# Kernel tuning notes

Measured on AMD Instinct MI355X. Metric: run time of the kernel, lower is better.

## Reference

```python
import jax, jax.numpy as jnp
import numpy as np

CUTOFF = 5.0
MAX_NBR = 32      # max_num_neighbors
LOOP = True
B, M = 128, 1024  # molecules, atoms per molecule (batch is uniform: batch[i] = i // M)
BOX = 26.0        # box side chosen so ~30 atoms fall within CUTOFF


def setup_inputs() -> dict:
    key = jax.random.key(0)
    pos = jax.random.uniform(key, (B * M, 3), dtype=jnp.float32) * BOX
    batch = jnp.repeat(jnp.arange(B, dtype=jnp.int32), M)
    return {"pos": pos, "batch": batch}


def reference(pos, batch):
    # radius_graph with per-graph (molecule) candidate search. Equal-size
    # molecules (batch = arange // M) let us use a dense [B, M, M] candidate
    # matrix per molecule; truncation keeps the K nearest within cutoff
    # (PyG keeps an arbitrary K within cutoff; nearest-K is the deterministic
    # variant). Output has fixed shape [2, B*M*K] padded with self-loops.
    posb = pos.reshape(B, M, 3)
    sq = jnp.sum(posb * posb, axis=-1)                       # [B, M]
    dot = jnp.einsum('bmd,bnd->bmn', posb, posb)             # [B, M, M]
    d2 = jnp.maximum(sq[:, :, None] + sq[:, None, :] - 2.0 * dot, 0.0)
    within = d2 <= CUTOFF * CUTOFF
    if not LOOP:
        within = within & ~jnp.eye(M, dtype=bool)[None]
    neg = jnp.where(within, -d2, -jnp.inf)
    vals, idx = jax.lax.top_k(neg, MAX_NBR)                  # [B, M, K]
    valid = jnp.isfinite(vals)
    center = jnp.arange(M, dtype=idx.dtype)[None, :, None]   # [1, M, 1]
    idx_eff = jnp.where(valid, idx, center)                  # pad invalid -> self

    b_ix = jnp.arange(B)[:, None, None]
    nbr = posb[b_ix, idx_eff]                                # [B, M, K, 3]
    edge_vec = nbr - posb[:, :, None, :]                     # pos[src] - pos[dst]

    is_self = idx_eff == center
    wmask = valid & ~is_self                                 # self-loops get weight 0
    d2sel = jnp.sum(edge_vec * edge_vec, axis=-1)
    edge_weight = jnp.where(wmask, jnp.sqrt(jnp.where(wmask, d2sel, 1.0)), 0.0)

    offs = (jnp.arange(B, dtype=idx.dtype) * M)[:, None, None]
    src = (offs + idx_eff).reshape(-1)                       # neighbor (edge_index[0])
    dst = jnp.broadcast_to(offs + center, (B, M, MAX_NBR)).reshape(-1)
    edge_index = jnp.stack([src, dst])                       # [2, B*M*K]
    return edge_index, edge_weight.reshape(-1), edge_vec.reshape(-1, 3)
```

## Files before the change

kernel.cpp:

```cpp
#include <hip/hip_runtime.h>

#define NB 128
#define NM 1024
#define NK 32
#define NS 16
#define CUT2 25.0f
#define CUT2_BITS 0x41C80000u
#define KEYMASK   0xFFFFFC00u

typedef unsigned int   u32;
typedef unsigned short u16;
typedef float vf4 __attribute__((ext_vector_type(4)));

__global__ __launch_bounds__(256) void pack_atoms(const float* __restrict__ pos,
                                                  float4* __restrict__ scanb,
                                                  float4* __restrict__ rawb, int dual)
{
  int i = blockIdx.x * 256 + threadIdx.x;
  float x = pos[3*i+0], y = pos[3*i+1], z = pos[3*i+2];
  float sq = x*x + y*y + z*z;
  rawb[i] = make_float4(x, y, z, sq);
  if (dual) scanb[i] = make_float4(-2.f*x, -2.f*y, -2.f*z, sq);
}

__device__ __forceinline__ void ce_asc(u32 &a, u32 &b) {
  u32 mn = a < b ? a : b;
  u32 mx = a < b ? b : a;
  a = mn; b = mx;
}

template <int N, int K, int D>
__device__ __forceinline__ void bitonic_pass(u32* r) {
#pragma unroll
  for (int i = 0; i < N; ++i)
    if ((i & D) == 0) {
      if ((i & K) == 0) ce_asc(r[i], r[i | D]);
      else              ce_asc(r[i | D], r[i]);
    }
}

template <bool NEG2>
__global__ __launch_bounds__(256, 4) void radius_knn(const float4* __restrict__ scanb,
                                                     const float4* __restrict__ rawb,
                                                     float* __restrict__ out)
{
  __shared__ float xs[NM], ys[NM], zs[NM], sqs[NM];
  __shared__ u32 lmem[4096];
  u16* lists = (u16*)lmem;

  const int tid  = threadIdx.x;
  const int lane = tid & 127;
  const int half = tid >> 7;
  const int molb = blockIdx.x & 127;
  const int q8   = blockIdx.x >> 7;
  const int c    = molb * NM + q8 * 128 + lane;
  const int mloc = c & (NM - 1);

  const float4* st = rawb + (size_t)molb * NM;
  for (int t = tid; t < NM; t += 256) {
    float4 a = st[t];
    xs[t] = a.x; ys[t] = a.y; zs[t] = a.z; sqs[t] = a.w;
  }
  __syncthreads();

  const float mex = xs[mloc], mey = ys[mloc], mez = zs[mloc], mew = sqs[mloc];

  const float4* mp = scanb + ((size_t)(c >> 10) << 10);
  const int jbase = half * 512;
  int cnt = 0;
  float4 ta[8], tb[8];
#pragma unroll
  for (int u = 0; u < 8; ++u) ta[u] = mp[jbase + u];

  auto body = [&](const float4* t, int j0) {
#pragma unroll
    for (int u = 0; u < 8; ++u) {
      float d2;
      if (NEG2) {
        d2 = __builtin_fmaf(mex, t[u].x,
             __builtin_fmaf(mey, t[u].y,
             __builtin_fmaf(mez, t[u].z, mew + t[u].w)));
      } else {
        float dot = (mex*t[u].x + mey*t[u].y) + mez*t[u].z;
        d2 = __builtin_fmaf(-2.f, dot, mew + t[u].w);
      }
      int slot = cnt < NS ? cnt : (NS - 1);
      lists[slot * 256 + tid] = (u16)(j0 + u);
      cnt += (d2 <= CUT2) ? 1 : 0;
    }
  };

  for (int g = 0; g < 64; g += 2) {
    const int j1 = jbase + (((g + 1) & 63) << 3);
#pragma unroll
    for (int u = 0; u < 8; ++u) tb[u] = mp[j1 + u];
    body(ta, jbase + (g << 3));
    const int j2 = jbase + (((g + 2) & 63) << 3);
#pragma unroll
    for (int u = 0; u < 8; ++u) ta[u] = mp[j2 + u];
    body(tb, jbase + ((g + 1) << 3));
  }
  if (cnt > NS) cnt = NS;

  const u32 PADK = 0x7F800000u | (u32)mloc;
  u32 r[NK];
#pragma unroll
  for (int k = 0; k < NS; ++k) {
    u32 key = PADK;
    if (k < cnt) {
      int j = lists[k * 256 + tid];
      float dot = (mex*xs[j] + mey*ys[j]) + mez*zs[j];
      float d2  = fmaxf((mew + sqs[j]) - 2.f*dot, 0.f);
      key = (__float_as_uint(d2) & KEYMASK) | (u32)j;
    }
    r[k] = key;
  }
  bitonic_pass<16, 2, 1>(r);
  bitonic_pass<16, 4, 2>(r); bitonic_pass<16, 4, 1>(r);
  bitonic_pass<16, 8, 4>(r); bitonic_pass<16, 8, 2>(r); bitonic_pass<16, 8, 1>(r);
  bitonic_pass<16,16, 8>(r); bitonic_pass<16,16, 4>(r); bitonic_pass<16,16, 2>(r); bitonic_pass<16,16, 1>(r);

  __syncthreads();
  {
    u32* myp = lmem + half * 2048 + lane * 16;
#pragma unroll
    for (int k = 0; k < NS; ++k) myp[(k + lane) & 15] = r[k];
  }
  __syncthreads();
  {
    u32* op = lmem + (1 - half) * 2048 + lane * 16;
#pragma unroll
    for (int i = 0; i < NS; ++i) r[16 + i] = op[((15 - i) + lane) & 15];
  }
  bitonic_pass<32,32,16>(r); bitonic_pass<32,32, 8>(r); bitonic_pass<32,32, 4>(r);
  bitonic_pass<32,32, 2>(r); bitonic_pass<32,32, 1>(r);

  const long long E = (long long)NB * NM * NK;
  const float base = (float)((c >> 10) * NM);

  if (!half) {
    vf4* ps = (vf4*)(out       + (size_t)c * NK);
    vf4* pd = (vf4*)(out +   E + (size_t)c * NK);
    vf4* pw = (vf4*)(out + 2*E + (size_t)c * NK);
    const float fc = (float)c;
    const vf4 dstv = {fc, fc, fc, fc};
#pragma unroll
    for (int q = 0; q < 8; ++q) {
      float sv[4], wv[4];
#pragma unroll
      for (int u = 0; u < 4; ++u) {
        u32 key = r[4*q + u];
        int idx = (int)(key & 1023u);
        bool valid = (key & KEYMASK) <= CUT2_BITS;
        float vx = xs[idx] - mex;
        float vy = ys[idx] - mey;
        float vz = zs[idx] - mez;
        bool wm  = valid && (idx != mloc);
        float d2s = vx*vx + vy*vy + vz*vz;
        wv[u] = wm ? sqrtf(d2s) : 0.0f;
        sv[u] = base + (float)idx;
      }
      ps[q] = (vf4){sv[0], sv[1], sv[2], sv[3]};
      pd[q] = dstv;
      pw[q] = (vf4){wv[0], wv[1], wv[2], wv[3]};
    }
  } else {
    vf4* pv = (vf4*)(out + 3*E + (size_t)c * NK * 3);
#pragma unroll
    for (int q = 0; q < 8; ++q) {
      float vv[12];
#pragma unroll
      for (int u = 0; u < 4; ++u) {
        int idx = (int)(r[4*q + u] & 1023u);
        vv[3*u+0] = xs[idx] - mex;
        vv[3*u+1] = ys[idx] - mey;
        vv[3*u+2] = zs[idx] - mez;
      }
      pv[3*q+0] = (vf4){vv[0], vv[1], vv[2],  vv[3]};
      pv[3*q+1] = (vf4){vv[4], vv[5], vv[6],  vv[7]};
      pv[3*q+2] = (vf4){vv[8], vv[9], vv[10], vv[11]};
    }
  }
}

extern "C" void kernel_launch(void* const* d_in, const int* in_sizes, int n_in,
                              void* d_out, int out_size, void* d_ws, size_t ws_size,
                              hipStream_t stream) {
  const float* pos = (const float*)d_in[0];
  float* out = (float*)d_out;
  const size_t one = (size_t)NB * NM * sizeof(float4);

  if (ws_size >= 2 * one) {
    float4* scanb = (float4*)d_ws;
    float4* rawb  = (float4*)((char*)d_ws + one);
    hipLaunchKernelGGL(pack_atoms, dim3((NB*NM)/256), dim3(256), 0, stream,
                       pos, scanb, rawb, 1);
    hipLaunchKernelGGL((radius_knn<true>), dim3(2*(NB*NM)/256), dim3(256), 0, stream,
                       scanb, rawb, out);
  } else {
    float4* rawb = (float4*)d_ws;
    hipLaunchKernelGGL(pack_atoms, dim3((NB*NM)/256), dim3(256), 0, stream,
                       pos, rawb, rawb, 0);
    hipLaunchKernelGGL((radius_knn<false>), dim3(2*(NB*NM)/256), dim3(256), 0, stream,
                       rawb, rawb, out);
  }
}
```

Measured before the change: 192.1 us.

## Drop raw atom buffer, stage prescaled float4 atoms in LDS, add sched barriers

The pack kernel now writes only the prescaled (-2x,-2y,-2z,|x|^2) buffer, and the main kernel loads that buffer into a float4 LDS array. It recovers raw coordinates by multiplying by -0.5, which halves the pack-kernel writes and removes the dual-buffer workspace path. LDS gathers become single 16-byte reads instead of four scalar reads from separate arrays. Scheduling barriers are added around the prefetch loads to keep loads issued ahead of compute. Edge vectors are now rebuilt from scaled values, which may change rounding slightly, and the barriers may limit compiler interleaving.

```diff
diff --git a/kernel.cpp b/kernel.cpp
--- a/kernel.cpp
+++ b/kernel.cpp
@@ -13,14 +13,12 @@
 typedef float vf4 __attribute__((ext_vector_type(4)));
 
 __global__ __launch_bounds__(256) void pack_atoms(const float* __restrict__ pos,
-                                                  float4* __restrict__ scanb,
-                                                  float4* __restrict__ rawb, int dual)
+                                                  float4* __restrict__ scanb)
 {
   int i = blockIdx.x * 256 + threadIdx.x;
   float x = pos[3*i+0], y = pos[3*i+1], z = pos[3*i+2];
   float sq = x*x + y*y + z*z;
-  rawb[i] = make_float4(x, y, z, sq);
-  if (dual) scanb[i] = make_float4(-2.f*x, -2.f*y, -2.f*z, sq);
+  scanb[i] = make_float4(-2.f*x, -2.f*y, -2.f*z, sq);
 }
 
 __device__ __forceinline__ void ce_asc(u32 &a, u32 &b) {
@@ -39,12 +37,10 @@
     }
 }
 
-template <bool NEG2>
 __global__ __launch_bounds__(256, 4) void radius_knn(const float4* __restrict__ scanb,
-                                                     const float4* __restrict__ rawb,
                                                      float* __restrict__ out)
 {
-  __shared__ float xs[NM], ys[NM], zs[NM], sqs[NM];
+  __shared__ float4 s4[NM];
   __shared__ u32 lmem[4096];
   u16* lists = (u16*)lmem;
 
@@ -56,14 +52,13 @@
   const int c    = molb * NM + q8 * 128 + lane;
   const int mloc = c & (NM - 1);
 
-  const float4* st = rawb + (size_t)molb * NM;
-  for (int t = tid; t < NM; t += 256) {
-    float4 a = st[t];
-    xs[t] = a.x; ys[t] = a.y; zs[t] = a.z; sqs[t] = a.w;
-  }
+  const float4* st = scanb + (size_t)molb * NM;
+  for (int t = tid; t < NM; t += 256) s4[t] = st[t];
   __syncthreads();
 
-  const float mex = xs[mloc], mey = ys[mloc], mez = zs[mloc], mew = sqs[mloc];
+  const float4 mc = s4[mloc];
+  const float mex = -0.5f * mc.x, mey = -0.5f * mc.y, mez = -0.5f * mc.z;
+  const float mew = mc.w;
 
   const float4* mp = scanb + ((size_t)(c >> 10) << 10);
   const int jbase = half * 512;
@@ -71,19 +66,14 @@
   float4 ta[8], tb[8];
 #pragma unroll
   for (int u = 0; u < 8; ++u) ta[u] = mp[jbase + u];
+  __builtin_amdgcn_sched_barrier(0);
 
   auto body = [&](const float4* t, int j0) {
 #pragma unroll
     for (int u = 0; u < 8; ++u) {
-      float d2;
-      if (NEG2) {
-        d2 = __builtin_fmaf(mex, t[u].x,
-             __builtin_fmaf(mey, t[u].y,
-             __builtin_fmaf(mez, t[u].z, mew + t[u].w)));
-      } else {
-        float dot = (mex*t[u].x + mey*t[u].y) + mez*t[u].z;
-        d2 = __builtin_fmaf(-2.f, dot, mew + t[u].w);
-      }
+      float d2 = __builtin_fmaf(mex, t[u].x,
+                 __builtin_fmaf(mey, t[u].y,
+                 __builtin_fmaf(mez, t[u].z, mew + t[u].w)));
       int slot = cnt < NS ? cnt : (NS - 1);
       lists[slot * 256 + tid] = (u16)(j0 + u);
       cnt += (d2 <= CUT2) ? 1 : 0;
@@ -94,10 +84,12 @@
     const int j1 = jbase + (((g + 1) & 63) << 3);
 #pragma unroll
     for (int u = 0; u < 8; ++u) tb[u] = mp[j1 + u];
+    __builtin_amdgcn_sched_barrier(0);
     body(ta, jbase + (g << 3));
     const int j2 = jbase + (((g + 2) & 63) << 3);
 #pragma unroll
     for (int u = 0; u < 8; ++u) ta[u] = mp[j2 + u];
+    __builtin_amdgcn_sched_barrier(0);
     body(tb, jbase + ((g + 1) << 3));
   }
   if (cnt > NS) cnt = NS;
@@ -109,8 +101,10 @@
     u32 key = PADK;
     if (k < cnt) {
       int j = lists[k * 256 + tid];
-      float dot = (mex*xs[j] + mey*ys[j]) + mez*zs[j];
-      float d2  = fmaxf((mew + sqs[j]) - 2.f*dot, 0.f);
+      float4 cj = s4[j];
+      float d2 = fmaxf(__builtin_fmaf(mex, cj.x,
+                  __builtin_fmaf(mey, cj.y,
+                  __builtin_fmaf(mez, cj.z, mew + cj.w))), 0.f);
       key = (__float_as_uint(d2) & KEYMASK) | (u32)j;
     }
     r[k] = key;
@@ -137,6 +131,7 @@
 
   const long long E = (long long)NB * NM * NK;
   const float base = (float)((c >> 10) * NM);
+  const float nmex = -mex, nmey = -mey, nmez = -mez;
 
   if (!half) {
     vf4* ps = (vf4*)(out       + (size_t)c * NK);
@@ -151,10 +146,11 @@
       for (int u = 0; u < 4; ++u) {
         u32 key = r[4*q + u];
         int idx = (int)(key & 1023u);
+        float4 cj = s4[idx];
         bool valid = (key & KEYMASK) <= CUT2_BITS;
-        float vx = xs[idx] - mex;
-        float vy = ys[idx] - mey;
-        float vz = zs[idx] - mez;
+        float vx = __builtin_fmaf(-0.5f, cj.x, nmex);
+        float vy = __builtin_fmaf(-0.5f, cj.y, nmey);
+        float vz = __builtin_fmaf(-0.5f, cj.z, nmez);
         bool wm  = valid && (idx != mloc);
         float d2s = vx*vx + vy*vy + vz*vz;
         wv[u] = wm ? sqrtf(d2s) : 0.0f;
@@ -172,9 +168,10 @@
 #pragma unroll
       for (int u = 0; u < 4; ++u) {
         int idx = (int)(r[4*q + u] & 1023u);
-        vv[3*u+0] = xs[idx] - mex;
-        vv[3*u+1] = ys[idx] - mey;
-        vv[3*u+2] = zs[idx] - mez;
+        float4 cj = s4[idx];
+        vv[3*u+0] = __builtin_fmaf(-0.5f, cj.x, nmex);
+        vv[3*u+1] = __builtin_fmaf(-0.5f, cj.y, nmey);
+        vv[3*u+2] = __builtin_fmaf(-0.5f, cj.z, nmez);
       }
       pv[3*q+0] = (vf4){vv[0], vv[1], vv[2],  vv[3]};
       pv[3*q+1] = (vf4){vv[4], vv[5], vv[6],  vv[7]};
@@ -188,20 +185,7 @@
                               hipStream_t stream) {
   const float* pos = (const float*)d_in[0];
   float* out = (float*)d_out;
-  const size_t one = (size_t)NB * NM * sizeof(float4);
-
-  if (ws_size >= 2 * one) {
-    float4* scanb = (float4*)d_ws;
-    float4* rawb  = (float4*)((char*)d_ws + one);
-    hipLaunchKernelGGL(pack_atoms, dim3((NB*NM)/256), dim3(256), 0, stream,
-                       pos, scanb, rawb, 1);
-    hipLaunchKernelGGL((radius_knn<true>), dim3(2*(NB*NM)/256), dim3(256), 0, stream,
-                       scanb, rawb, out);
-  } else {
-    float4* rawb = (float4*)d_ws;
-    hipLaunchKernelGGL(pack_atoms, dim3((NB*NM)/256), dim3(256), 0, stream,
-                       pos, rawb, rawb, 0);
-    hipLaunchKernelGGL((radius_knn<false>), dim3(2*(NB*NM)/256), dim3(256), 0, stream,
-                       rawb, rawb, out);
-  }
+  float4* scanb = (float4*)d_ws;
+  hipLaunchKernelGGL(pack_atoms, dim3((NB*NM)/256), dim3(256), 0, stream, pos, scanb);
+  hipLaunchKernelGGL(radius_knn, dim3(2*(NB*NM)/256), dim3(256), 0, stream, scanb, out);
 }
```

After: 187.2 us. -2.5%, faster.
